# Optimization experiments

Hardware: AMD Instinct MI355X
Metric: run time of the kernel (lower is better)

The kernel has to match this reference:

```python
import jax, jax.numpy as jnp
import numpy as np

D_MODEL = 2048
D_INNER = 2048
N_QK = 32
N_V = 32
D_STATE = 64
D_CONV = 4
CHUNK = 128
CONV_DIM = D_INNER + 2 * N_QK * D_STATE  # 6144
IN_OUT = 2 * D_INNER + 2 * N_QK * D_STATE + N_V  # 8224


def setup_inputs() -> dict:
    key = jax.random.key(0)
    ks = jax.random.split(key, 6)
    u = jax.random.normal(ks[0], (2, 4096, D_MODEL), dtype=jnp.float32)
    W_in = jax.random.normal(ks[1], (IN_OUT, D_MODEL), dtype=jnp.float32) * 0.02
    conv_w = jax.random.normal(ks[2], (CONV_DIM, D_CONV), dtype=jnp.float32) * 0.2
    conv_b = jax.random.normal(ks[3], (CONV_DIM,), dtype=jnp.float32) * 0.02
    D = jnp.ones((N_V,), dtype=jnp.float32)
    z_bias = jnp.zeros((D_INNER,), dtype=jnp.float32)
    W_out = jax.random.normal(ks[4], (D_MODEL, D_INNER), dtype=jnp.float32) * 0.02
    return {"u": u, "W_in": W_in, "conv_w": conv_w, "conv_b": conv_b,
            "D": D, "z_bias": z_bias, "W_out": W_out}


def causal_depthwise_conv(x, w, b):
    # x: [B, L, C]; w: [C, K]; b: [C]. Torch Conv1d(groups=C, padding=K-1)[..., :L]
    B, L, C = x.shape
    K = w.shape[1]
    xp = jnp.pad(x, ((0, 0), (K - 1, 0), (0, 0)))
    y = b[None, None, :]
    for k in range(K):
        y = y + xp[:, k:k + L, :] * w[None, None, :, k]
    return y


def ssd_chunk_scan(x, dt, B, C, chunk):
    # Mamba2 SSD with A = -1 per head.
    # x: [b,l,h,p], dt: [b,l,h] (positive), B,C: [b,l,h,n]
    b, l, h, p = x.shape
    n = B.shape[-1]
    nc = l // chunk
    x = x.reshape(b, nc, chunk, h, p)
    dt = dt.reshape(b, nc, chunk, h)
    B = B.reshape(b, nc, chunk, h, n)
    C = C.reshape(b, nc, chunk, h, n)
    a = -dt                                  # A * dt
    cum = jnp.cumsum(a, axis=2)              # [b,nc,q,h]
    xdt = x * dt[..., None]                  # dt_t * x_t
    # ---- intra-chunk (causal, decay exp(cum_q - cum_k), q >= k) ----
    CB = jnp.einsum('bcqhn,bckhn->bchqk', C, B)
    cumT = jnp.swapaxes(cum, 2, 3)           # [b,nc,h,q]
    diff = cumT[..., :, None] - cumT[..., None, :]   # [b,nc,h,q,k]
    mask = jnp.tril(jnp.ones((chunk, chunk), dtype=bool))
    decay = jnp.exp(jnp.where(mask, diff, -jnp.inf))
    y_intra = jnp.einsum('bchqk,bckhp->bcqhp', CB * decay, xdt)
    # ---- per-chunk final states ----
    state_decay = jnp.exp(cum[:, :, -1:, :] - cum)   # [b,nc,q,h]
    states = jnp.einsum('bckhn,bckhp->bchpn', B * state_decay[..., None], xdt)
    chunk_decay = jnp.exp(cum[:, :, -1, :])          # [b,nc,h]
    # ---- inter-chunk recurrence ----
    def step(carry, inp):
        st, cd = inp  # st [b,h,p,n], cd [b,h]
        new = carry * cd[:, :, None, None] + st
        return new, carry  # emit the state *entering* this chunk
    init = jnp.zeros((b, h, p, n), dtype=x.dtype)
    _, prev = jax.lax.scan(step, init,
                           (jnp.moveaxis(states, 1, 0), jnp.moveaxis(chunk_decay, 1, 0)))
    prev = jnp.moveaxis(prev, 0, 1)                  # [b,nc,h,p,n]
    y_inter = jnp.einsum('bcqhn,bchpn->bcqhp', C * jnp.exp(cum)[..., None], prev)
    return (y_intra + y_inter).reshape(b, l, h, p)


def reference(u, W_in, conv_w, conv_b, D, z_bias, W_out):
    b, l, _ = u.shape  # l divisible by CHUNK (padded_len == l)
    xBCzA = jnp.einsum('bld,od->blo', u, W_in)
    xBC = xBCzA[..., :CONV_DIM]
    z = xBCzA[..., CONV_DIM:CONV_DIM + D_INNER]
    A_log = xBCzA[..., CONV_DIM + D_INNER:]
    xBC = causal_depthwise_conv(xBC, conv_w, conv_b)  # activation = identity
    x = xBC[..., :D_INNER]
    Bm = xBC[..., D_INNER:D_INNER + N_QK * D_STATE]
    Cm = xBC[..., D_INNER + N_QK * D_STATE:]
    x = x.reshape(b, l, N_V, D_INNER // N_V)
    Bm = Bm.reshape(b, l, N_QK, D_STATE)
    Cm = Cm.reshape(b, l, N_QK, D_STATE)
    dt = jax.nn.softplus(A_log)                       # [b,l,h]
    x_scan = x / dt[..., None]
    y = ssd_chunk_scan(x_scan, dt, Bm, Cm, CHUNK)
    y = y + D[None, None, :, None] * x                # Du uses undivided x
    y = y.reshape(b, l, D_INNER)
    out = jnp.einsum('bli,oi->blo', y * jax.nn.silu(z + z_bias), W_out)
    return out
```

## Files before the change

kernel.cpp:

```cpp
#include <hip/hip_runtime.h>
#include <math.h>

#define D_MODEL  2048
#define D_INNER  2048
#define N_QK     32
#define N_V      32
#define D_STATE  64
#define D_CONV   4
#define CHUNK    128
#define CONV_DIM 6144
#define IN_OUT   8224
#define BATCH    2
#define SEQ      4096
#define M_ROWS   (BATCH*SEQ)
#define NCHUNK   (SEQ/CHUNK)

typedef unsigned short bf16_t;
typedef __attribute__((ext_vector_type(4))) float f32x4;
typedef __attribute__((ext_vector_type(8))) short bf16x8;

#define SWZ64(r,c)  ((((r)*64)  + (c)) ^ (((r)&7)<<3))
#define SWZ128(r,c) ((((r)*128) + (c)) ^ (((r)&7)<<3))

__device__ __forceinline__ float b2f(bf16_t u) {
    union { unsigned int i; float f; } w; w.i = ((unsigned int)u) << 16; return w.f;
}
__device__ __forceinline__ bf16_t f2b(float f) {
    unsigned int x = __float_as_uint(f);
    return (bf16_t)((x + 0x7FFFu + ((x >> 16) & 1u)) >> 16);
}
__device__ __forceinline__ void store4b(bf16_t* dst, float4 v) {
    ushort4 u; u.x = f2b(v.x); u.y = f2b(v.y); u.z = f2b(v.z); u.w = f2b(v.w);
    *reinterpret_cast<ushort4*>(dst) = u;
}

__device__ __forceinline__ void gload_lds16(const bf16_t* g, bf16_t* l) {
    __builtin_amdgcn_global_load_lds((const __attribute__((address_space(1))) void*)g,
                                     (__attribute__((address_space(3))) void*)l,
                                     16, 0, 0);
}

__global__ __launch_bounds__(256) void f2b3_kernel(const float* __restrict__ a0, bf16_t* __restrict__ o0, long n0,
                                                   const float* __restrict__ a1, bf16_t* __restrict__ o1, long n1,
                                                   const float* __restrict__ a2, bf16_t* __restrict__ o2, long n2)
{
    const long total = (n0 + n1 + n2) >> 2;
    for (long s = (long)blockIdx.x * 256 + threadIdx.x; s < total; s += (long)gridDim.x * 256) {
        long i = s << 2;
        const float* in; bf16_t* out;
        if (i < n0)           { in = a0 + i; out = o0 + i; }
        else if (i < n0 + n1) { i -= n0; in = a1 + i; out = o1 + i; }
        else                  { i -= n0 + n1; in = a2 + i; out = o2 + i; }
        float4 v = *reinterpret_cast<const float4*>(in);
        ushort4 o;
        o.x = f2b(v.x); o.y = f2b(v.y); o.z = f2b(v.z); o.w = f2b(v.w);
        *reinterpret_cast<ushort4*>(out) = o;
    }
}

template<int NTB, int K, bool OBF16>
__global__ __launch_bounds__(512, 2) void gemm256(const bf16_t* __restrict__ A,
                                                  const bf16_t* __restrict__ B,
                                                  void* __restrict__ Cv,
                                                  long ldc)
{
    constexpr int BK = 64;
    constexpr int NT = K / BK;
    __shared__ bf16_t As[2][2][8192];
    __shared__ bf16_t Bs[2][2][8192];

    const int nwg = gridDim.x;
    const int bid = blockIdx.x;
    const int wg  = ((nwg & 7) == 0) ? ((bid & 7) * (nwg >> 3) + (bid >> 3)) : bid;
    const int bm = (wg / NTB) * 256;
    const int bn = (wg % NTB) * 256;

    const int tid  = threadIdx.x;
    const int lane = tid & 63;
    const int wv   = tid >> 6;
    const int wr   = wv >> 2, wc = wv & 3;
    const int l15  = lane & 15, l4 = lane >> 4;

    f32x4 acc[8][4];
    #pragma unroll
    for (int i = 0; i < 8; ++i)
        #pragma unroll
        for (int j = 0; j < 4; ++j) acc[i][j] = (f32x4){0.f, 0.f, 0.f, 0.f};

    const bf16_t* Abase = A + (long)bm * K;
    const bf16_t* Bbase = B + (long)bn * K;

    auto stage_half = [&](int t, int buf, int kh) {
        #pragma unroll
        for (int it = 0; it < 2; ++it) {
            const int s   = it * 512 + tid;
            const int row = s >> 2;
            const int jp  = s & 3;
            const int jl  = jp ^ ((row >> 1) & 3);
            const long go = (long)row * K + t * BK + kh * 32 + jl * 8;
            gload_lds16(Abase + go, &As[buf][kh][s * 8]);
            gload_lds16(Bbase + go, &Bs[buf][kh][s * 8]);
        }
    };
    auto rdA = [&](int buf, int kh, int row) {
        const int jp = l4 ^ ((row >> 1) & 3);
        return *reinterpret_cast<const bf16x8*>(&As[buf][kh][(row * 4 + jp) * 8]);
    };
    auto rdB = [&](int buf, int kh, int row) {
        const int jp = l4 ^ ((row >> 1) & 3);
        return *reinterpret_cast<const bf16x8*>(&Bs[buf][kh][(row * 4 + jp) * 8]);
    };

    stage_half(0, 0, 0);
    stage_half(0, 0, 1);
    asm volatile("s_waitcnt vmcnt(4)" ::: "memory");
    __builtin_amdgcn_s_barrier();

    for (int t = 0; t < NT; ++t) {
        const int cur = t & 1;
        bf16x8 bfr[4], af[4];
        if (t + 1 < NT) stage_half(t + 1, cur ^ 1, 0);
        #pragma unroll
        for (int ni = 0; ni < 4; ++ni) bfr[ni] = rdB(cur, 0, wc * 64 + ni * 16 + l15);
        #pragma unroll
        for (int mi = 0; mi < 4; ++mi) af[mi] = rdA(cur, 0, wr * 128 + mi * 16 + l15);
        __builtin_amdgcn_s_setprio(1);
        #pragma unroll
        for (int mi = 0; mi < 4; ++mi)
            #pragma unroll
            for (int ni = 0; ni < 4; ++ni)
                acc[mi][ni] = __builtin_amdgcn_mfma_f32_16x16x32_bf16(
                    af[mi], bfr[ni], acc[mi][ni], 0, 0, 0);
        __builtin_amdgcn_s_setprio(0);
        #pragma unroll
        for (int mi = 0; mi < 4; ++mi) af[mi] = rdA(cur, 0, wr * 128 + 64 + mi * 16 + l15);
        __builtin_amdgcn_s_setprio(1);
        #pragma unroll
        for (int mi = 0; mi < 4; ++mi)
            #pragma unroll
            for (int ni = 0; ni < 4; ++ni)
                acc[4 + mi][ni] = __builtin_amdgcn_mfma_f32_16x16x32_bf16(
                    af[mi], bfr[ni], acc[4 + mi][ni], 0, 0, 0);
        __builtin_amdgcn_s_setprio(0);
        if (t + 1 < NT) {
            stage_half(t + 1, cur ^ 1, 1);
            asm volatile("s_waitcnt vmcnt(8)" ::: "memory");
        } else {
            asm volatile("s_waitcnt vmcnt(0)" ::: "memory");
        }
        __builtin_amdgcn_s_barrier();
        #pragma unroll
        for (int ni = 0; ni < 4; ++ni) bfr[ni] = rdB(cur, 1, wc * 64 + ni * 16 + l15);
        #pragma unroll
        for (int mi = 0; mi < 4; ++mi) af[mi] = rdA(cur, 1, wr * 128 + mi * 16 + l15);
        __builtin_amdgcn_s_setprio(1);
        #pragma unroll
        for (int mi = 0; mi < 4; ++mi)
            #pragma unroll
            for (int ni = 0; ni < 4; ++ni)
                acc[mi][ni] = __builtin_amdgcn_mfma_f32_16x16x32_bf16(
                    af[mi], bfr[ni], acc[mi][ni], 0, 0, 0);
        __builtin_amdgcn_s_setprio(0);
        #pragma unroll
        for (int mi = 0; mi < 4; ++mi) af[mi] = rdA(cur, 1, wr * 128 + 64 + mi * 16 + l15);
        __builtin_amdgcn_s_setprio(1);
        #pragma unroll
        for (int mi = 0; mi < 4; ++mi)
            #pragma unroll
            for (int ni = 0; ni < 4; ++ni)
                acc[4 + mi][ni] = __builtin_amdgcn_mfma_f32_16x16x32_bf16(
                    af[mi], bfr[ni], acc[4 + mi][ni], 0, 0, 0);
        __builtin_amdgcn_s_setprio(0);
        if (t + 1 < NT) { asm volatile("s_waitcnt vmcnt(4)" ::: "memory"); }
        __builtin_amdgcn_s_barrier();
    }

    #pragma unroll
    for (int mf = 0; mf < 8; ++mf) {
        const long grow0 = bm + wr * 128 + mf * 16 + l4 * 4;
        #pragma unroll
        for (int ni = 0; ni < 4; ++ni) {
            const int gcol = bn + wc * 64 + ni * 16 + l15;
            #pragma unroll
            for (int j = 0; j < 4; ++j) {
                if (OBF16)
                    ((bf16_t*)Cv)[(grow0 + j) * ldc + gcol] = f2b(acc[mf][ni][j]);
                else
                    ((float*)Cv)[(grow0 + j) * ldc + gcol] = acc[mf][ni][j];
            }
        }
    }
}

__global__ __launch_bounds__(256) void alog_partial(const bf16_t* __restrict__ A,
                                                    const bf16_t* __restrict__ Bt,
                                                    float* __restrict__ P)
{
    const int rb = blockIdx.x & 63, ks = blockIdx.x >> 6;
    const int bm = rb * 128;
    __shared__ bf16_t As[128 * 64];
    __shared__ bf16_t Bs[32 * 64];
    const int tid = threadIdx.x, lane = tid & 63, wv = tid >> 6;
    const int l15 = lane & 15, l4 = lane >> 4;

    f32x4 acc[2][2];
    #pragma unroll
    for (int mi = 0; mi < 2; ++mi)
        #pragma unroll
        for (int nj = 0; nj < 2; ++nj) acc[mi][nj] = (f32x4){0.f, 0.f, 0.f, 0.f};

    for (int it8 = 0; it8 < 8; ++it8) {
        const long kbase = (long)ks * 512 + it8 * 64;
        #pragma unroll
        for (int it = 0; it < 4; ++it) {
            const int s = it * 256 + tid;
            const int row = s >> 3, c16 = s & 7;
            gload_lds16(A + (long)(bm + row) * D_MODEL + kbase + (c16 ^ (row & 7)) * 8,
                        &As[s * 8]);
        }
        {
            const int row = tid >> 3, c16 = tid & 7;
            gload_lds16(Bt + (long)row * D_MODEL + kbase + (c16 ^ (row & 7)) * 8,
                        &Bs[tid * 8]);
        }
        __syncthreads();
        #pragma unroll
        for (int kk = 0; kk < 2; ++kk) {
            bf16x8 bf[2], af;
            #pragma unroll
            for (int nj = 0; nj < 2; ++nj) {
                const int row = nj * 16 + l15;
                bf[nj] = *reinterpret_cast<const bf16x8*>(&Bs[row * 64 + (((kk * 4 + l4) ^ (row & 7)) << 3)]);
            }
            #pragma unroll
            for (int mi = 0; mi < 2; ++mi) {
                const int row = wv * 32 + mi * 16 + l15;
                af = *reinterpret_cast<const bf16x8*>(&As[row * 64 + (((kk * 4 + l4) ^ (row & 7)) << 3)]);
                #pragma unroll
                for (int nj = 0; nj < 2; ++nj)
                    acc[mi][nj] = __builtin_amdgcn_mfma_f32_16x16x32_bf16(af, bf[nj], acc[mi][nj], 0, 0, 0);
            }
        }
        __syncthreads();
    }
    #pragma unroll
    for (int mi = 0; mi < 2; ++mi)
        #pragma unroll
        for (int nj = 0; nj < 2; ++nj)
            #pragma unroll
            for (int j = 0; j < 4; ++j) {
                const int row = bm + wv * 32 + mi * 16 + l4 * 4 + j;
                P[(long)ks * (M_ROWS * 32) + (long)row * 32 + nj * 16 + l15] = acc[mi][nj][j];
            }
}

__device__ __forceinline__ float4 conv4v(const bf16_t* __restrict__ xb, long m, int l,
                                         int col, const float* __restrict__ cw,
                                         const float* __restrict__ cbv)
{
    float4 acc = *reinterpret_cast<const float4*>(cbv + col);
    float4 wc0 = *reinterpret_cast<const float4*>(cw + (long)col * 4);
    float4 wc1 = *reinterpret_cast<const float4*>(cw + (long)col * 4 + 4);
    float4 wc2 = *reinterpret_cast<const float4*>(cw + (long)col * 4 + 8);
    float4 wc3 = *reinterpret_cast<const float4*>(cw + (long)col * 4 + 12);
    const float t0[4] = {wc0.x, wc0.y, wc0.z, wc0.w};
    const float t1[4] = {wc1.x, wc1.y, wc1.z, wc1.w};
    const float t2[4] = {wc2.x, wc2.y, wc2.z, wc2.w};
    const float t3[4] = {wc3.x, wc3.y, wc3.z, wc3.w};
    #pragma unroll
    for (int tap = 0; tap < 4; ++tap) {
        if (l - 3 + tap < 0) continue;
        const bf16_t* p = xb + (m - 3 + tap) * (long)IN_OUT + col;
        ushort4 v = *reinterpret_cast<const ushort4*>(p);
        acc.x = fmaf(b2f(v.x), t0[tap], acc.x);
        acc.y = fmaf(b2f(v.y), t1[tap], acc.y);
        acc.z = fmaf(b2f(v.z), t2[tap], acc.z);
        acc.w = fmaf(b2f(v.w), t3[tap], acc.w);
    }
    return acc;
}

template<int EXPL>
__global__ __launch_bounds__(512, 6) void ssd_states(const bf16_t* __restrict__ xb,
                                                     const float* __restrict__ P,
                                                     const float* __restrict__ cw,
                                                     const float* __restrict__ cbv,
                                                     bf16_t* __restrict__ states,
                                                     float* __restrict__ cumbuf,
                                                     float* __restrict__ cdecay,
                                                     bf16_t* __restrict__ xtg,
                                                     bf16_t* __restrict__ bg,
                                                     bf16_t* __restrict__ cg)
{
    const int h = blockIdx.x, c = blockIdx.y, b = blockIdx.z;
    __shared__ bf16_t sx [128 * 64];
    __shared__ bf16_t sBr[128 * 64];
    __shared__ bf16_t sC [128 * 64];
    __shared__ float  cum[CHUNK];
    __shared__ float  w0tot;
    const int t = threadIdx.x;
    const long mbase = (long)b * SEQ + (long)c * CHUNK;
    const long cb = ((long)b * NCHUNK + c) * N_QK + h;

    float v = 0.f;
    if (t < CHUNK) {
        const long n = (long)M_ROWS * 32;
        const long pi = (mbase + t) * N_V + h;
        const float a = P[pi] + P[n + pi] + P[2 * n + pi] + P[3 * n + pi];
        v = -((a > 20.f) ? a : log1pf(expf(a)));
        #pragma unroll
        for (int s = 1; s < 64; s <<= 1) {
            const float u2 = __shfl_up(v, s, 64);
            if ((t & 63) >= s) v += u2;
        }
        if (t == 63) w0tot = v;
    }
    for (int idx = t; idx < CHUNK * 16; idx += 512) {
        const int k = idx >> 4, q4 = (idx & 15) * 4;
        const long m = mbase + k;
        const int l = (int)(m & (SEQ - 1));
        float4 xv = conv4v(xb, m, l, h * 64 + q4, cw, cbv);
        float4 bv = conv4v(xb, m, l, D_INNER + h * 64 + q4, cw, cbv);
        store4b(&sx [SWZ64(k, q4)], xv);
        store4b(&sBr[SWZ64(k, q4)], bv);
        if (EXPL == 2) {
            float4 cv = conv4v(xb, m, l, 2 * D_INNER + h * 64 + q4, cw, cbv);
            store4b(&sC[SWZ64(k, q4)], cv);
        }
    }
    __syncthreads();
    if (t >= 64 && t < CHUNK) v += w0tot;
    if (t < CHUNK) cum[t] = v;
    const int j = t & 127;
    const int c8b = (t >> 7) * 2;
    bf16x8 rx[2], rb[2];
    #pragma unroll
    for (int it = 0; it < 2; ++it) {
        rx[it] = *reinterpret_cast<const bf16x8*>(&sx [SWZ64(j, (c8b + it) * 8)]);
        rb[it] = *reinterpret_cast<const bf16x8*>(&sBr[SWZ64(j, (c8b + it) * 8)]);
    }
    if (EXPL >= 1) {
        #pragma unroll
        for (int it = 0; it < 2; ++it) {
            const int s = it * 512 + t;
            *reinterpret_cast<bf16x8*>(bg + cb * 8192 + s * 8) =
                *reinterpret_cast<const bf16x8*>(&sBr[s * 8]);
            if (EXPL == 2)
                *reinterpret_cast<bf16x8*>(cg + cb * 8192 + s * 8) =
                    *reinterpret_cast<const bf16x8*>(&sC[s * 8]);
        }
    }
    __syncthreads();
    const float clast = cum[CHUNK - 1];
    const float ej = __expf(clast - cum[j]);
    #pragma unroll
    for (int it = 0; it < 2; ++it) {
        const int c8 = c8b + it;
        #pragma unroll
        for (int e = 0; e < 8; ++e) {
            sx [SWZ128(c8 * 8 + e, j)] = rx[it][e];
            sBr[SWZ128(c8 * 8 + e, j)] = f2b(b2f((bf16_t)rb[it][e]) * ej);
        }
    }
    __syncthreads();

    if (EXPL >= 1) {
        #pragma unroll
        for (int it = 0; it < 2; ++it) {
            const int s = it * 512 + t;
            *reinterpret_cast<bf16x8*>(xtg + cb * 8192 + s * 8) =
                *reinterpret_cast<const bf16x8*>(&sx[s * 8]);
        }
    }

    const int lane = t & 63, wv = t >> 6;
    const int l15 = lane & 15, l4 = lane >> 4;
    const int prow  = (wv & 3) * 16;
    const int nbase = (wv >> 2) * 2;
    f32x4 acc[2];
    acc[0] = (f32x4){0.f, 0.f, 0.f, 0.f};
    acc[1] = (f32x4){0.f, 0.f, 0.f, 0.f};
    #pragma unroll
    for (int ks = 0; ks < 4; ++ks) {
        const int kc = ks * 32 + l4 * 8;
        bf16x8 af = *reinterpret_cast<const bf16x8*>(&sx[SWZ128(prow + l15, kc)]);
        #pragma unroll
        for (int nj = 0; nj < 2; ++nj) {
            bf16x8 bf = *reinterpret_cast<const bf16x8*>(&sBr[SWZ128((nbase + nj) * 16 + l15, kc)]);
            acc[nj] = __builtin_amdgcn_mfma_f32_16x16x32_bf16(af, bf, acc[nj], 0, 0, 0);
        }
    }
    #pragma unroll
    for (int nj = 0; nj < 2; ++nj) {
        #pragma unroll
        for (int jj = 0; jj < 4; ++jj) {
            const int p = prow + l4 * 4 + jj;
            states[cb * 4096 + SWZ64(p, (nbase + nj) * 16 + l15)] = f2b(acc[nj][jj]);
        }
    }
    if (t < CHUNK) cumbuf[cb * CHUNK + t] = cum[t];
    if (t == 0)   cdecay[cb] = __expf(clast);
}

__global__ __launch_bounds__(256) void ssd_scan(bf16_t* __restrict__ states,
                                                const float* __restrict__ cdecay)
{
    const int bid = blockIdx.x;
    const int bh = bid >> 3, q = bid & 7;
    const int b = bh >> 5, h = bh & 31;
    const int t = threadIdx.x;
    __shared__ bf16_t sst[NCHUNK * 512];
    __shared__ float  scd[NCHUNK];
    if (t < NCHUNK) scd[t] = cdecay[((long)b * NCHUNK + t) * N_QK + h];
    #pragma unroll
    for (int it = 0; it < 8; ++it) {
        const int slot = it * 256 + t;
        const int c = slot >> 6, off = (slot & 63) * 8;
        const long g = (((long)b * NCHUNK + c) * N_QK + h) * 4096 + q * 512 + off;
        gload_lds16(states + g, &sst[slot * 8]);
    }
    __syncthreads();
    float2 carry = make_float2(0.f, 0.f);
    for (int c = 0; c < NCHUNK; ++c) {
        ushort2* p = reinterpret_cast<ushort2*>(&sst[c * 512 + t * 2]);
        const ushort2 su = *p;
        ushort2 pv;
        pv.x = f2b(carry.x); pv.y = f2b(carry.y);
        *p = pv;
        const float cd = scd[c];
        carry.x = fmaf(carry.x, cd, b2f(su.x));
        carry.y = fmaf(carry.y, cd, b2f(su.y));
    }
    __syncthreads();
    #pragma unroll
    for (int it = 0; it < 8; ++it) {
        const int slot = it * 256 + t;
        const int c = slot >> 6, off = (slot & 63) * 8;
        const long g = (((long)b * NCHUNK + c) * N_QK + h) * 4096 + q * 512 + off;
        *reinterpret_cast<bf16x8*>(states + g) =
            *reinterpret_cast<const bf16x8*>(&sst[slot * 8]);
    }
}

template<int EXPL>
__global__ __launch_bounds__(512, 4) void ssd_out(const bf16_t* __restrict__ xb,
                                                  const float* __restrict__ cumbuf,
                                                  const bf16_t* __restrict__ prevst,
                                                  const float* __restrict__ Dvec,
                                                  const float* __restrict__ zbias,
                                                  const float* __restrict__ cw,
                                                  const float* __restrict__ cbv,
                                                  const bf16_t* __restrict__ xtg,
                                                  const bf16_t* __restrict__ bg,
                                                  const bf16_t* __restrict__ cg,
                                                  bf16_t* __restrict__ yz)
{
    const int h = blockIdx.x, c = blockIdx.y, b = blockIdx.z;
    __shared__ bf16_t sC[128 * 64];
    __shared__ bf16_t sB[128 * 64];
    __shared__ bf16_t sXQ[128 * 64];
    __shared__ bf16_t sXT[64 * 128];
    __shared__ bf16_t sP[64 * 64];
    __shared__ float  cum[CHUNK];
    const int t = threadIdx.x;
    const long mbase = (long)b * SEQ + (long)c * CHUNK;
    const long cb = ((long)b * NCHUNK + c) * N_QK + h;
    if (t < CHUNK) cum[t] = cumbuf[cb * CHUNK + t];
    gload_lds16(prevst + cb * 4096 + t * 8, &sP[t * 8]);
    if (EXPL == 2) {
        #pragma unroll
        for (int it = 0; it < 2; ++it) {
            const int s = it * 512 + t;
            gload_lds16(bg  + cb * 8192 + s * 8, &sB [s * 8]);
            gload_lds16(xtg + cb * 8192 + s * 8, &sXT[s * 8]);
            gload_lds16(cg  + cb * 8192 + s * 8, &sC [s * 8]);
        }
        __syncthreads();
    } else if (EXPL == 1) {
        #pragma unroll
        for (int it = 0; it < 2; ++it) {
            const int s = it * 512 + t;
            gload_lds16(bg  + cb * 8192 + s * 8, &sB [s * 8]);
            gload_lds16(xtg + cb * 8192 + s * 8, &sXT[s * 8]);
        }
        for (int idx = t; idx < CHUNK * 16; idx += 512) {
            const int k = idx >> 4, q4 = (idx & 15) * 4;
            const long m = mbase + k;
            const int l = (int)(m & (SEQ - 1));
            float4 cv = conv4v(xb, m, l, 2 * D_INNER + h * 64 + q4, cw, cbv);
            store4b(&sC[SWZ64(k, q4)], cv);
        }
        __syncthreads();
    } else {
        for (int idx = t; idx < CHUNK * 16; idx += 512) {
            const int k = idx >> 4, q4 = (idx & 15) * 4;
            const long m = mbase + k;
            const int l = (int)(m & (SEQ - 1));
            float4 xv = conv4v(xb, m, l, h * 64 + q4, cw, cbv);
            float4 bv = conv4v(xb, m, l, D_INNER + h * 64 + q4, cw, cbv);
            float4 cv = conv4v(xb, m, l, 2 * D_INNER + h * 64 + q4, cw, cbv);
            store4b(&sXQ[SWZ64(k, q4)], xv);
            store4b(&sB [SWZ64(k, q4)], bv);
            store4b(&sC [SWZ64(k, q4)], cv);
        }
        __syncthreads();
        {
            const int j = t & 127;
            const int c8b = (t >> 7) * 2;
            #pragma unroll
            for (int it = 0; it < 2; ++it) {
                const int c8 = c8b + it;
                bf16x8 v = *reinterpret_cast<const bf16x8*>(&sXQ[SWZ64(j, c8 * 8)]);
                #pragma unroll
                for (int e = 0; e < 8; ++e) sXT[SWZ128(c8 * 8 + e, j)] = v[e];
            }
        }
        __syncthreads();
    }

    const int lane = t & 63, wv = t >> 6;
    const int w16 = wv * 16, l15 = lane & 15, l4 = lane >> 4;
    bf16_t* sQ = sXQ;

    f32x4 yac[4], iac[4];
    #pragma unroll
    for (int np = 0; np < 4; ++np) {
        yac[np] = (f32x4){0.f, 0.f, 0.f, 0.f};
        iac[np] = (f32x4){0.f, 0.f, 0.f, 0.f};
    }

    #pragma unroll
    for (int H = 0; H < 2; ++H) {
        if (H == 1 && wv < 4) break;
        const int j0 = H * 64;
        f32x4 sac[4];
        #pragma unroll
        for (int nj = 0; nj < 4; ++nj) sac[nj] = (f32x4){0.f, 0.f, 0.f, 0.f};
        #pragma unroll
        for (int kk = 0; kk < 2; ++kk) {
            const int kc = kk * 32 + l4 * 8;
            bf16x8 af0 = *reinterpret_cast<const bf16x8*>(&sC[SWZ64(w16 + l15, kc)]);
            #pragma unroll
            for (int nj = 0; nj < 4; ++nj) {
                if (j0 + nj * 16 <= w16 + 15) {
                    bf16x8 bfj = *reinterpret_cast<const bf16x8*>(&sB[SWZ64(j0 + nj * 16 + l15, kc)]);
                    sac[nj] = __builtin_amdgcn_mfma_f32_16x16x32_bf16(af0, bfj, sac[nj], 0, 0, 0);
                }
            }
        }
        #pragma unroll
        for (int nj = 0; nj < 4; ++nj) {
            const int jcol = nj * 16 + l15;
            const int jg = j0 + jcol;
            #pragma unroll
            for (int jj = 0; jj < 4; ++jj) {
                const int i = w16 + l4 * 4 + jj;
                const float q = (jg <= i) ? __expf(cum[i] - cum[jg]) * sac[nj][jj] : 0.f;
                sQ[SWZ64(i, jcol)] = f2b(q);
            }
        }
        #pragma unroll
        for (int kk = 0; kk < 2; ++kk) {
            const int kc = kk * 32 + l4 * 8;
            bf16x8 qa = *reinterpret_cast<const bf16x8*>(&sQ[SWZ64(w16 + l15, kc)]);
            #pragma unroll
            for (int np = 0; np < 4; ++np) {
                bf16x8 xf = *reinterpret_cast<const bf16x8*>(&sXT[SWZ128(np * 16 + l15, j0 + kc)]);
                yac[np] = __builtin_amdgcn_mfma_f32_16x16x32_bf16(qa, xf, yac[np], 0, 0, 0);
            }
        }
    }
    #pragma unroll
    for (int kk = 0; kk < 2; ++kk) {
        const int kc = kk * 32 + l4 * 8;
        bf16x8 cf = *reinterpret_cast<const bf16x8*>(&sC[SWZ64(w16 + l15, kc)]);
        #pragma unroll
        for (int np = 0; np < 4; ++np) {
            bf16x8 pf = *reinterpret_cast<const bf16x8*>(&sP[SWZ64(np * 16 + l15, kc)]);
            iac[np] = __builtin_amdgcn_mfma_f32_16x16x32_bf16(cf, pf, iac[np], 0, 0, 0);
        }
    }
    const float dh = Dvec[h];
    #pragma unroll
    for (int jj = 0; jj < 4; ++jj) {
        const int i = w16 + l4 * 4 + jj;
        const float ei = __expf(cum[i]);
        const long m = mbase + i;
        const bf16_t* zr = xb + m * (long)IN_OUT + CONV_DIM + h * 64;
        bf16_t* orow = yz + m * (long)D_INNER + h * 64;
        #pragma unroll
        for (int np = 0; np < 4; ++np) {
            const int p = np * 16 + l15;
            const float xval = b2f(sXT[SWZ128(p, i)]);
            const float y = yac[np][jj] + ei * iac[np][jj] + dh * xval;
            const float zv = b2f(zr[p]) + zbias[h * 64 + p];
            const float s = zv / (1.f + __expf(-zv));
            orow[p] = f2b(y * s);
        }
    }
}

extern "C" void kernel_launch(void* const* d_in, const int* in_sizes, int n_in,
                              void* d_out, int out_size, void* d_ws, size_t ws_size,
                              hipStream_t stream)
{
    const float* u      = (const float*)d_in[0];
    const float* W_in   = (const float*)d_in[1];
    const float* conv_w = (const float*)d_in[2];
    const float* conv_b = (const float*)d_in[3];
    const float* Dv     = (const float*)d_in[4];
    const float* z_bias = (const float*)d_in[5];
    const float* W_out  = (const float*)d_in[6];
    float* out = (float*)d_out;

    char* w = (char*)d_ws;
    bf16_t* xbcza = (bf16_t*)w;  w += (long)M_ROWS * IN_OUT * 2;
    bf16_t* wob   = (bf16_t*)w;  w += (long)2048 * 2048 * 2;
    char* ureg = w;  w += 67239936;
    bf16_t* ub  = (bf16_t*)ureg;
    bf16_t* wib = (bf16_t*)(ureg + (long)M_ROWS * D_MODEL * 2);
    bf16_t* yzb = (bf16_t*)ureg;
    float*  cumb   = (float*)(ureg + (long)M_ROWS * D_INNER * 2);
    bf16_t* states = (bf16_t*)(cumb + (long)BATCH * NCHUNK * N_QK * CHUNK);
    float*  cdec   = (float*)(states + (long)BATCH * NCHUNK * N_QK * 4096);
    float* partials = (float*)(ureg + 58720256);
    const long base_bytes = (long)(w - (char*)d_ws);
    const long exp1_bytes = 2L * 2048 * 8192 * 2;
    const long exp2_bytes = 3L * 2048 * 8192 * 2;
    const int expl = ((long)ws_size >= base_bytes + exp2_bytes) ? 2
                   : ((long)ws_size >= base_bytes + exp1_bytes) ? 1 : 0;
    bf16_t* xtg = (bf16_t*)w;
    bf16_t* bg  = xtg + (long)2048 * 8192;
    bf16_t* cg  = bg  + (long)2048 * 8192;

    {
        const long n0 = (long)M_ROWS * D_MODEL;
        const long n1 = (long)IN_OUT * D_MODEL;
        const long n2 = (long)D_MODEL * D_INNER;
        f2b3_kernel<<<2048, 256, 0, stream>>>(u, ub, n0, W_in, wib, n1, W_out, wob, n2);
    }

    gemm256<32, D_MODEL, true><<<(M_ROWS / 256) * 32, 512, 0, stream>>>(
        ub, wib, xbcza, IN_OUT);

    alog_partial<<<256, 256, 0, stream>>>(ub, wib + (long)8192 * D_MODEL, partials);

    dim3 sg(N_QK, NCHUNK, BATCH);
    if (expl == 2) {
        ssd_states<2><<<sg, 512, 0, stream>>>(xbcza, partials, conv_w, conv_b,
                                              states, cumb, cdec, xtg, bg, cg);
        ssd_scan<<<BATCH * N_QK * 8, 256, 0, stream>>>(states, cdec);
        ssd_out<2><<<sg, 512, 0, stream>>>(xbcza, cumb, states, Dv, z_bias,
                                           conv_w, conv_b, xtg, bg, cg, yzb);
    } else if (expl == 1) {
        ssd_states<1><<<sg, 512, 0, stream>>>(xbcza, partials, conv_w, conv_b,
                                              states, cumb, cdec, xtg, bg, nullptr);
        ssd_scan<<<BATCH * N_QK * 8, 256, 0, stream>>>(states, cdec);
        ssd_out<1><<<sg, 512, 0, stream>>>(xbcza, cumb, states, Dv, z_bias,
                                           conv_w, conv_b, xtg, bg, nullptr, yzb);
    } else {
        ssd_states<0><<<sg, 512, 0, stream>>>(xbcza, partials, conv_w, conv_b,
                                              states, cumb, cdec, nullptr, nullptr, nullptr);
        ssd_scan<<<BATCH * N_QK * 8, 256, 0, stream>>>(states, cdec);
        ssd_out<0><<<sg, 512, 0, stream>>>(xbcza, cumb, states, Dv, z_bias,
                                           conv_w, conv_b, nullptr, nullptr, nullptr, yzb);
    }

    gemm256<8, D_INNER, false><<<(M_ROWS / 256) * 8, 512, 0, stream>>>(
        yzb, wob, out, D_MODEL);
}
```

Baseline: 708.9 us.

## Slim ssd_out LDS footprint by reusing C buffer and reading prev states from global

Adds a specialized ssd_out_s kernel for the precomputed-operand paths. It drops the separate sP and sXQ shared buffers, scales C by exp(cum) in place, and reuses the same buffer for the masked decay matrix. The previous chunk state is read straight from global memory as MFMA fragments. Launch bounds are raised from 4 to 6 blocks per CU to increase occupancy, which raises register pressure and adds in-place LDS reuse that needs careful ordering. The conv-from-scratch path moves to a separate ssd_out0 kernel.

```diff
diff --git a/kernel.cpp b/kernel.cpp
--- a/kernel.cpp
+++ b/kernel.cpp
@@ -443,17 +443,169 @@
 }
 
 template<int EXPL>
-__global__ __launch_bounds__(512, 4) void ssd_out(const bf16_t* __restrict__ xb,
-                                                  const float* __restrict__ cumbuf,
-                                                  const bf16_t* __restrict__ prevst,
-                                                  const float* __restrict__ Dvec,
-                                                  const float* __restrict__ zbias,
-                                                  const float* __restrict__ cw,
-                                                  const float* __restrict__ cbv,
-                                                  const bf16_t* __restrict__ xtg,
-                                                  const bf16_t* __restrict__ bg,
-                                                  const bf16_t* __restrict__ cg,
-                                                  bf16_t* __restrict__ yz)
+__global__ __launch_bounds__(512, 6) void ssd_out_s(const bf16_t* __restrict__ xb,
+                                                    const float* __restrict__ cumbuf,
+                                                    const bf16_t* __restrict__ prevst,
+                                                    const float* __restrict__ Dvec,
+                                                    const float* __restrict__ zbias,
+                                                    const float* __restrict__ cw,
+                                                    const float* __restrict__ cbv,
+                                                    const bf16_t* __restrict__ xtg,
+                                                    const bf16_t* __restrict__ bg,
+                                                    const bf16_t* __restrict__ cg,
+                                                    bf16_t* __restrict__ yz)
+{
+    const int h = blockIdx.x, c = blockIdx.y, b = blockIdx.z;
+    __shared__ bf16_t sB [128 * 64];
+    __shared__ bf16_t sCQ[128 * 64];
+    __shared__ bf16_t sXT[64 * 128];
+    __shared__ float  cum[CHUNK];
+    const int t = threadIdx.x;
+    const long mbase = (long)b * SEQ + (long)c * CHUNK;
+    const long cb = ((long)b * NCHUNK + c) * N_QK + h;
+    if (t < CHUNK) cum[t] = cumbuf[cb * CHUNK + t];
+    #pragma unroll
+    for (int it = 0; it < 2; ++it) {
+        const int s = it * 512 + t;
+        gload_lds16(bg  + cb * 8192 + s * 8, &sB [s * 8]);
+        gload_lds16(xtg + cb * 8192 + s * 8, &sXT[s * 8]);
+        if (EXPL == 2) gload_lds16(cg + cb * 8192 + s * 8, &sCQ[s * 8]);
+    }
+    if (EXPL == 1) {
+        for (int idx = t; idx < CHUNK * 16; idx += 512) {
+            const int k = idx >> 4, q4 = (idx & 15) * 4;
+            const long m = mbase + k;
+            const int l = (int)(m & (SEQ - 1));
+            float4 cv = conv4v(xb, m, l, 2 * D_INNER + h * 64 + q4, cw, cbv);
+            store4b(&sCQ[SWZ64(k, q4)], cv);
+        }
+    }
+    __syncthreads();
+
+    const int lane = t & 63, wv = t >> 6;
+    const int w16 = wv * 16, l15 = lane & 15, l4 = lane >> 4;
+
+    f32x4 sacA[4], sacB[4];
+    #pragma unroll
+    for (int nj = 0; nj < 4; ++nj) {
+        sacA[nj] = (f32x4){0.f, 0.f, 0.f, 0.f};
+        sacB[nj] = (f32x4){0.f, 0.f, 0.f, 0.f};
+    }
+    #pragma unroll
+    for (int kk = 0; kk < 2; ++kk) {
+        const int kc = kk * 32 + l4 * 8;
+        bf16x8 af0 = *reinterpret_cast<const bf16x8*>(&sCQ[SWZ64(w16 + l15, kc)]);
+        #pragma unroll
+        for (int nj = 0; nj < 4; ++nj) {
+            if (nj * 16 <= w16 + 15) {
+                bf16x8 bfj = *reinterpret_cast<const bf16x8*>(&sB[SWZ64(nj * 16 + l15, kc)]);
+                sacA[nj] = __builtin_amdgcn_mfma_f32_16x16x32_bf16(af0, bfj, sacA[nj], 0, 0, 0);
+            }
+        }
+        if (wv >= 4) {
+            #pragma unroll
+            for (int nj = 0; nj < 4; ++nj) {
+                if (64 + nj * 16 <= w16 + 15) {
+                    bf16x8 bfj = *reinterpret_cast<const bf16x8*>(&sB[SWZ64(64 + nj * 16 + l15, kc)]);
+                    sacB[nj] = __builtin_amdgcn_mfma_f32_16x16x32_bf16(af0, bfj, sacB[nj], 0, 0, 0);
+                }
+            }
+        }
+    }
+    #pragma unroll
+    for (int jj = 0; jj < 4; ++jj) {
+        const int i = w16 + l4 * 4 + jj;
+        const float ei = __expf(cum[i]);
+        ushort4* pc = reinterpret_cast<ushort4*>(&sCQ[SWZ64(i, l15 * 4)]);
+        ushort4 cv = *pc;
+        cv.x = f2b(b2f(cv.x) * ei); cv.y = f2b(b2f(cv.y) * ei);
+        cv.z = f2b(b2f(cv.z) * ei); cv.w = f2b(b2f(cv.w) * ei);
+        *pc = cv;
+    }
+    f32x4 yac[4];
+    #pragma unroll
+    for (int np = 0; np < 4; ++np) yac[np] = (f32x4){0.f, 0.f, 0.f, 0.f};
+    #pragma unroll
+    for (int kk = 0; kk < 2; ++kk) {
+        const int kc = kk * 32 + l4 * 8;
+        bf16x8 cf = *reinterpret_cast<const bf16x8*>(&sCQ[SWZ64(w16 + l15, kc)]);
+        #pragma unroll
+        for (int np = 0; np < 4; ++np) {
+            bf16x8 pf = *reinterpret_cast<const bf16x8*>(
+                prevst + cb * 4096 + SWZ64(np * 16 + l15, kc));
+            yac[np] = __builtin_amdgcn_mfma_f32_16x16x32_bf16(cf, pf, yac[np], 0, 0, 0);
+        }
+    }
+    #pragma unroll
+    for (int nj = 0; nj < 4; ++nj) {
+        const int jcol = nj * 16 + l15;
+        #pragma unroll
+        for (int jj = 0; jj < 4; ++jj) {
+            const int i = w16 + l4 * 4 + jj;
+            const float q = (jcol <= i) ? __expf(cum[i] - cum[jcol]) * sacA[nj][jj] : 0.f;
+            sCQ[SWZ64(i, jcol)] = f2b(q);
+        }
+    }
+    #pragma unroll
+    for (int kk = 0; kk < 2; ++kk) {
+        const int kc = kk * 32 + l4 * 8;
+        bf16x8 qa = *reinterpret_cast<const bf16x8*>(&sCQ[SWZ64(w16 + l15, kc)]);
+        #pragma unroll
+        for (int np = 0; np < 4; ++np) {
+            bf16x8 xf = *reinterpret_cast<const bf16x8*>(&sXT[SWZ128(np * 16 + l15, kc)]);
+            yac[np] = __builtin_amdgcn_mfma_f32_16x16x32_bf16(qa, xf, yac[np], 0, 0, 0);
+        }
+    }
+    if (wv >= 4) {
+        #pragma unroll
+        for (int nj = 0; nj < 4; ++nj) {
+            const int jcol = nj * 16 + l15;
+            const int jg = 64 + jcol;
+            #pragma unroll
+            for (int jj = 0; jj < 4; ++jj) {
+                const int i = w16 + l4 * 4 + jj;
+                const float q = (jg <= i) ? __expf(cum[i] - cum[jg]) * sacB[nj][jj] : 0.f;
+                sCQ[SWZ64(i, jcol)] = f2b(q);
+            }
+        }
+        #pragma unroll
+        for (int kk = 0; kk < 2; ++kk) {
+            const int kc = kk * 32 + l4 * 8;
+            bf16x8 qa = *reinterpret_cast<const bf16x8*>(&sCQ[SWZ64(w16 + l15, kc)]);
+            #pragma unroll
+            for (int np = 0; np < 4; ++np) {
+                bf16x8 xf = *reinterpret_cast<const bf16x8*>(&sXT[SWZ128(np * 16 + l15, 64 + kc)]);
+                yac[np] = __builtin_amdgcn_mfma_f32_16x16x32_bf16(qa, xf, yac[np], 0, 0, 0);
+            }
+        }
+    }
+    const float dh = Dvec[h];
+    #pragma unroll
+    for (int jj = 0; jj < 4; ++jj) {
+        const int i = w16 + l4 * 4 + jj;
+        const long m = mbase + i;
+        const bf16_t* zr = xb + m * (long)IN_OUT + CONV_DIM + h * 64;
+        bf16_t* orow = yz + m * (long)D_INNER + h * 64;
+        #pragma unroll
+        for (int np = 0; np < 4; ++np) {
+            const int p = np * 16 + l15;
+            const float xval = b2f(sXT[SWZ128(p, i)]);
+            const float y = yac[np][jj] + dh * xval;
+            const float zv = b2f(zr[p]) + zbias[h * 64 + p];
+            const float s = zv / (1.f + __expf(-zv));
+            orow[p] = f2b(y * s);
+        }
+    }
+}
+
+__global__ __launch_bounds__(512, 4) void ssd_out0(const bf16_t* __restrict__ xb,
+                                                   const float* __restrict__ cumbuf,
+                                                   const bf16_t* __restrict__ prevst,
+                                                   const float* __restrict__ Dvec,
+                                                   const float* __restrict__ zbias,
+                                                   const float* __restrict__ cw,
+                                                   const float* __restrict__ cbv,
+                                                   bf16_t* __restrict__ yz)
 {
     const int h = blockIdx.x, c = blockIdx.y, b = blockIdx.z;
     __shared__ bf16_t sC[128 * 64];
@@ -467,56 +619,30 @@
     const long cb = ((long)b * NCHUNK + c) * N_QK + h;
     if (t < CHUNK) cum[t] = cumbuf[cb * CHUNK + t];
     gload_lds16(prevst + cb * 4096 + t * 8, &sP[t * 8]);
-    if (EXPL == 2) {
+    for (int idx = t; idx < CHUNK * 16; idx += 512) {
+        const int k = idx >> 4, q4 = (idx & 15) * 4;
+        const long m = mbase + k;
+        const int l = (int)(m & (SEQ - 1));
+        float4 xv = conv4v(xb, m, l, h * 64 + q4, cw, cbv);
+        float4 bv = conv4v(xb, m, l, D_INNER + h * 64 + q4, cw, cbv);
+        float4 cv = conv4v(xb, m, l, 2 * D_INNER + h * 64 + q4, cw, cbv);
+        store4b(&sXQ[SWZ64(k, q4)], xv);
+        store4b(&sB [SWZ64(k, q4)], bv);
+        store4b(&sC [SWZ64(k, q4)], cv);
+    }
+    __syncthreads();
+    {
+        const int j = t & 127;
+        const int c8b = (t >> 7) * 2;
         #pragma unroll
         for (int it = 0; it < 2; ++it) {
-            const int s = it * 512 + t;
-            gload_lds16(bg  + cb * 8192 + s * 8, &sB [s * 8]);
-            gload_lds16(xtg + cb * 8192 + s * 8, &sXT[s * 8]);
-            gload_lds16(cg  + cb * 8192 + s * 8, &sC [s * 8]);
-        }
-        __syncthreads();
-    } else if (EXPL == 1) {
-        #pragma unroll
-        for (int it = 0; it < 2; ++it) {
-            const int s = it * 512 + t;
-            gload_lds16(bg  + cb * 8192 + s * 8, &sB [s * 8]);
-            gload_lds16(xtg + cb * 8192 + s * 8, &sXT[s * 8]);
-        }
-        for (int idx = t; idx < CHUNK * 16; idx += 512) {
-            const int k = idx >> 4, q4 = (idx & 15) * 4;
-            const long m = mbase + k;
-            const int l = (int)(m & (SEQ - 1));
-            float4 cv = conv4v(xb, m, l, 2 * D_INNER + h * 64 + q4, cw, cbv);
-            store4b(&sC[SWZ64(k, q4)], cv);
-        }
-        __syncthreads();
-    } else {
-        for (int idx = t; idx < CHUNK * 16; idx += 512) {
-            const int k = idx >> 4, q4 = (idx & 15) * 4;
-            const long m = mbase + k;
-            const int l = (int)(m & (SEQ - 1));
-            float4 xv = conv4v(xb, m, l, h * 64 + q4, cw, cbv);
-            float4 bv = conv4v(xb, m, l, D_INNER + h * 64 + q4, cw, cbv);
-            float4 cv = conv4v(xb, m, l, 2 * D_INNER + h * 64 + q4, cw, cbv);
-            store4b(&sXQ[SWZ64(k, q4)], xv);
-            store4b(&sB [SWZ64(k, q4)], bv);
-            store4b(&sC [SWZ64(k, q4)], cv);
-        }
-        __syncthreads();
-        {
-            const int j = t & 127;
-            const int c8b = (t >> 7) * 2;
-            #pragma unroll
-            for (int it = 0; it < 2; ++it) {
-                const int c8 = c8b + it;
-                bf16x8 v = *reinterpret_cast<const bf16x8*>(&sXQ[SWZ64(j, c8 * 8)]);
-                #pragma unroll
-                for (int e = 0; e < 8; ++e) sXT[SWZ128(c8 * 8 + e, j)] = v[e];
-            }
-        }
-        __syncthreads();
-    }
+            const int c8 = c8b + it;
+            bf16x8 v = *reinterpret_cast<const bf16x8*>(&sXQ[SWZ64(j, c8 * 8)]);
+            #pragma unroll
+            for (int e = 0; e < 8; ++e) sXT[SWZ128(c8 * 8 + e, j)] = v[e];
+        }
+    }
+    __syncthreads();
 
     const int lane = t & 63, wv = t >> 6;
     const int w16 = wv * 16, l15 = lane & 15, l4 = lane >> 4;
@@ -650,20 +776,20 @@
         ssd_states<2><<<sg, 512, 0, stream>>>(xbcza, partials, conv_w, conv_b,
                                               states, cumb, cdec, xtg, bg, cg);
         ssd_scan<<<BATCH * N_QK * 8, 256, 0, stream>>>(states, cdec);
-        ssd_out<2><<<sg, 512, 0, stream>>>(xbcza, cumb, states, Dv, z_bias,
-                                           conv_w, conv_b, xtg, bg, cg, yzb);
+        ssd_out_s<2><<<sg, 512, 0, stream>>>(xbcza, cumb, states, Dv, z_bias,
+                                             conv_w, conv_b, xtg, bg, cg, yzb);
     } else if (expl == 1) {
         ssd_states<1><<<sg, 512, 0, stream>>>(xbcza, partials, conv_w, conv_b,
                                               states, cumb, cdec, xtg, bg, nullptr);
         ssd_scan<<<BATCH * N_QK * 8, 256, 0, stream>>>(states, cdec);
-        ssd_out<1><<<sg, 512, 0, stream>>>(xbcza, cumb, states, Dv, z_bias,
-                                           conv_w, conv_b, xtg, bg, nullptr, yzb);
+        ssd_out_s<1><<<sg, 512, 0, stream>>>(xbcza, cumb, states, Dv, z_bias,
+                                             conv_w, conv_b, xtg, bg, nullptr, yzb);
     } else {
         ssd_states<0><<<sg, 512, 0, stream>>>(xbcza, partials, conv_w, conv_b,
                                               states, cumb, cdec, nullptr, nullptr, nullptr);
         ssd_scan<<<BATCH * N_QK * 8, 256, 0, stream>>>(states, cdec);
-        ssd_out<0><<<sg, 512, 0, stream>>>(xbcza, cumb, states, Dv, z_bias,
-                                           conv_w, conv_b, nullptr, nullptr, nullptr, yzb);
+        ssd_out0<<<sg, 512, 0, stream>>>(xbcza, cumb, states, Dv, z_bias,
+                                         conv_w, conv_b, yzb);
     }
 
     gemm256<8, D_INNER, false><<<(M_ROWS / 256) * 8, 512, 0, stream>>>(
```

Result: no change. 709.4 us (+0.1%).
